# Optimization experiments

Hardware: AMD Instinct MI355X
Metric: run time of the kernel (lower is better)

Reference implementation:

```python
import jax, jax.numpy as jnp
import numpy as np

B, S, D, H, MEL = 64, 512, 512, 8, 80
HD = D // H  # head dim


def _lstm_cell(x, h, c, w_ih, w_hh, b_ih, b_hh):
    # torch gate order: i, f, g, o
    gates = x @ w_ih.T + h @ w_hh.T + b_ih + b_hh
    i, f, g, o = jnp.split(gates, 4, axis=-1)
    c = jax.nn.sigmoid(f) * c + jax.nn.sigmoid(i) * jnp.tanh(g)
    h = jax.nn.sigmoid(o) * jnp.tanh(c)
    return h, c


def setup_inputs() -> dict:
    key = jax.random.key(0)
    ks = jax.random.split(key, 24)
    s = 0.05
    inp = {"encoder_output": jax.random.normal(ks[0], (B, S, D), jnp.float32)}
    # MultiheadAttention params (torch layout: in_proj [3D, D])
    inp["attn_in_w"] = jax.random.normal(ks[1], (3 * D, D), jnp.float32) * s
    inp["attn_in_b"] = jax.random.normal(ks[2], (3 * D,), jnp.float32) * s
    inp["attn_out_w"] = jax.random.normal(ks[3], (D, D), jnp.float32) * s
    inp["attn_out_b"] = jax.random.normal(ks[4], (D,), jnp.float32) * s
    # LSTM1 (2 layers)
    names = [("l1_w_ih0", (4 * D, D)), ("l1_w_hh0", (4 * D, D)), ("l1_b_ih0", (4 * D,)), ("l1_b_hh0", (4 * D,)),
             ("l1_w_ih1", (4 * D, D)), ("l1_w_hh1", (4 * D, D)), ("l1_b_ih1", (4 * D,)), ("l1_b_hh1", (4 * D,)),
             ("l2_w_ih", (4 * D, D)), ("l2_w_hh", (4 * D, D)), ("l2_b_ih", (4 * D,)), ("l2_b_hh", (4 * D,)),
             ("proj_w", (MEL, D)), ("proj_b", (MEL,))]
    for i, (n, shp) in enumerate(names):
        inp[n] = jax.random.normal(ks[5 + i], shp, jnp.float32) * s
    return inp


def reference(encoder_output, attn_in_w, attn_in_b, attn_out_w, attn_out_b,
              l1_w_ih0, l1_w_hh0, l1_b_ih0, l1_b_hh0,
              l1_w_ih1, l1_w_hh1, l1_b_ih1, l1_b_hh1,
              l2_w_ih, l2_w_hh, l2_b_ih, l2_b_hh, proj_w, proj_b):
    b, s, d = encoder_output.shape
    max_len = s * 5
    wq, wk, wv = jnp.split(attn_in_w, 3, axis=0)
    bq, bk, bv = jnp.split(attn_in_b, 3, axis=0)
    # Precompute K, V over encoder output: [B, S, H, HD]
    K = (encoder_output @ wk.T + bk).reshape(b, s, H, HD)
    V = (encoder_output @ wv.T + bv).reshape(b, s, H, HD)
    scale = 1.0 / np.sqrt(HD)

    def attend(x):  # x: [B, D] single-token query
        q = ((x @ wq.T + bq) * scale).reshape(b, H, HD)
        scores = jnp.einsum('bhd,bshd->bhs', q, K)
        w = jax.nn.softmax(scores, axis=-1)
        ctx = jnp.einsum('bhs,bshd->bhd', w, V).reshape(b, d)
        return ctx @ attn_out_w.T + attn_out_b

    zeros = jnp.zeros((b, d), encoder_output.dtype)
    carry0 = (zeros, zeros, zeros, zeros, zeros, zeros, zeros)

    def step(carry, _):
        h10, c10, h11, c11, h2, c2, dec_in = carry
        h10, c10 = _lstm_cell(dec_in, h10, c10, l1_w_ih0, l1_w_hh0, l1_b_ih0, l1_b_hh0)
        h11, c11 = _lstm_cell(h10, h11, c11, l1_w_ih1, l1_w_hh1, l1_b_ih1, l1_b_hh1)
        attn_out = attend(h11)
        h2, c2 = _lstm_cell(attn_out, h2, c2, l2_w_ih, l2_w_hh, l2_b_ih, l2_b_hh)
        out = h2 @ proj_w.T + proj_b  # [B, MEL]
        return (h10, c10, h11, c11, h2, c2, h2), out

    _, ys = jax.lax.scan(step, carry0, None, length=max_len)
    return jnp.transpose(ys, (1, 0, 2))  # [B, max_len, MEL]
```

## Files before the change

kernel.cpp:

```cpp
#include <hip/hip_runtime.h>
#include <hip/hip_bf16.h>
#include <hip/hip_fp8.h>

#define DEV_INLINE __device__ __forceinline__

typedef __attribute__((ext_vector_type(8))) short bf16x8;
typedef __attribute__((ext_vector_type(4))) float f32x4;
typedef __attribute__((ext_vector_type(2))) float f32x2;
typedef __attribute__((ext_vector_type(4))) unsigned int u32x4;
typedef unsigned long long ull;

constexpr int Bc = 64, Sc = 512, Dc = 512, Hc = 8, HDc = 64, MELc = 80, Tc = 2560;
constexpr int OUTSTRIDE = Tc * MELc;

constexpr size_t SZ_KP8 = 64ull * 8 * 512 * 64;
constexpr size_t SZ_VP  = 64ull * 8 * 512 * 64 * 2;
constexpr size_t SZ_PL  = 128ull * 2048 * 16;
constexpr size_t OFF_KP8 = 0;
constexpr size_t OFF_VP  = OFF_KP8 + SZ_KP8;
constexpr size_t OFF_PL0 = OFF_VP + SZ_VP;
constexpr size_t OFF_PL1 = OFF_PL0 + SZ_PL;
constexpr size_t OFF_PL2 = OFF_PL1 + SZ_PL;
constexpr size_t OFF_PWQ = OFF_PL2 + SZ_PL;
constexpr size_t OFF_PP  = OFF_PWQ + 524288;
constexpr size_t OFF_BL0 = OFF_PP + 81920;
constexpr size_t OFF_BL1 = OFF_BL0 + 8192;
constexpr size_t OFF_BL2 = OFF_BL1 + 8192;
constexpr size_t OFF_B2E = OFF_BL2 + 8192;
constexpr size_t OFF_W2E = OFF_B2E + 8192;
constexpr size_t OFF_WOT = OFF_W2E + 2097152;
constexpr size_t OFF_ACT = OFF_WOT + 1048576;
constexpr size_t OFF_FLG = OFF_ACT + 524288;

constexpr unsigned DYN_LDS = 137344;

DEV_INLINE float bf2f(short s) { return __uint_as_float(((unsigned)(unsigned short)s) << 16); }
DEV_INLINE short f2bf(float f) { union { __hip_bfloat16 h; short s; } u; u.h = __float2bfloat16(f); return u.s; }
DEV_INLINE float sig_f(float x) { return 1.0f / (1.0f + __expf(-x)); }
DEV_INLINE float tanh_f(float x) {
  float ax = fabsf(x);
  float e = __expf(fminf(2.0f * ax, 80.0f));
  float r = 1.0f - 2.0f / (e + 1.0f);
  return copysignf(r, x);
}
DEV_INLINE bf16x8 cvt8(const float* p) {
  bf16x8 r;
#pragma unroll
  for (int i = 0; i < 8; ++i) r[i] = f2bf(p[i]);
  return r;
}
DEV_INLINE float fp8tof(unsigned v) {
  __hip_fp8_e4m3 t; t.__x = (__hip_fp8_storage_t)v; return (float)t;
}

template <bool HI>
DEV_INLINE f32x2 cvt2_fp8(unsigned w) {
#if defined(__has_builtin) && __has_builtin(__builtin_amdgcn_cvt_pk_f32_fp8)
  return __builtin_amdgcn_cvt_pk_f32_fp8(w, HI);
#else
  unsigned b = HI ? (w >> 16) : w;
  f32x2 r; r[0] = fp8tof(b & 0xFFu); r[1] = fp8tof((b >> 8) & 0xFFu);
  return r;
#endif
}

DEV_INLINE ull ld_dev_u64(const void* p) {
  return __hip_atomic_load((const ull*)p, __ATOMIC_RELAXED, __HIP_MEMORY_SCOPE_AGENT);
}
DEV_INLINE void st_dev_u64(void* p, ull v) {
  __hip_atomic_store((ull*)p, v, __ATOMIC_RELAXED, __HIP_MEMORY_SCOPE_AGENT);
}
DEV_INLINE bf16x8 ld_frag(const __hip_bfloat16* p) {
  union { bf16x8 v; ull u[2]; } r;
  r.u[0] = ld_dev_u64(p);
  r.u[1] = ld_dev_u64((const char*)p + 8);
  return r.v;
}

__global__ __launch_bounds__(256) void gemm_setup(const float* __restrict__ A,
                                                  const float* __restrict__ Bt,
                                                  const float* __restrict__ bias,
                                                  __hip_bfloat16* __restrict__ dst,
                                                  unsigned char* __restrict__ dst8,
                                                  int mode) {
  int tid = threadIdx.x, lane = tid & 63, wv = tid >> 6;
  int m0 = blockIdx.y * 64 + wv * 16;
  int nb = blockIdx.x * 64;
  int mrow = m0 + (lane & 15);
  int kb = (lane >> 4) * 8;
  f32x4 acc0 = {0,0,0,0}, acc1 = {0,0,0,0}, acc2 = {0,0,0,0}, acc3 = {0,0,0,0};
  const float* arow = A + (size_t)mrow * 512 + kb;
  const float* b0r = Bt + (size_t)(nb + 0 * 16 + (lane & 15)) * 512 + kb;
  const float* b1r = Bt + (size_t)(nb + 1 * 16 + (lane & 15)) * 512 + kb;
  const float* b2r = Bt + (size_t)(nb + 2 * 16 + (lane & 15)) * 512 + kb;
  const float* b3r = Bt + (size_t)(nb + 3 * 16 + (lane & 15)) * 512 + kb;
  for (int kk = 0; kk < 16; ++kk) {
    bf16x8 af = cvt8(arow + kk * 32);
    acc0 = __builtin_amdgcn_mfma_f32_16x16x32_bf16(af, cvt8(b0r + kk * 32), acc0, 0, 0, 0);
    acc1 = __builtin_amdgcn_mfma_f32_16x16x32_bf16(af, cvt8(b1r + kk * 32), acc1, 0, 0, 0);
    acc2 = __builtin_amdgcn_mfma_f32_16x16x32_bf16(af, cvt8(b2r + kk * 32), acc2, 0, 0, 0);
    acc3 = __builtin_amdgcn_mfma_f32_16x16x32_bf16(af, cvt8(b3r + kk * 32), acc3, 0, 0, 0);
  }
  int col16 = lane & 15, r0 = (lane >> 4) * 4;
  f32x4 accs[4] = {acc0, acc1, acc2, acc3};
#pragma unroll
  for (int nt = 0; nt < 4; ++nt) {
    int n = nb + nt * 16 + col16;
#pragma unroll
    for (int r = 0; r < 4; ++r) {
      int m = m0 + r0 + r;
      float v = accs[nt][r];
      if (mode == 0) {
        v += bias[n];
        int bb = m >> 9, s = m & 511, h = n >> 6, d = n & 63;
        dst[(((size_t)(bb * 8 + h) * 512 + s) * 64) + d] = __float2bfloat16(v);
      } else if (mode == 2) {
        v += bias[n];
        int bb = m >> 9, s = m & 511, h = n >> 6, d = n & 63;
        __hip_fp8_e4m3 q(v);
        dst8[(((size_t)(bb * 8 + h) * 512 + s) * 64) + d] = (unsigned char)q.__x;
      } else {
        dst[(size_t)m * 512 + n] = __float2bfloat16(v);
      }
    }
  }
}

__global__ __launch_bounds__(256) void transpose512(const float* __restrict__ in, float* __restrict__ out) {
  __shared__ float tl[32][33];
  int x = threadIdx.x & 31, ty = threadIdx.x >> 5;
  int bx = blockIdx.x * 32, by = blockIdx.y * 32;
#pragma unroll
  for (int r = 0; r < 4; ++r) tl[ty + r * 8][x] = in[(size_t)(by + ty + r * 8) * 512 + bx + x];
  __syncthreads();
#pragma unroll
  for (int r = 0; r < 4; ++r) out[(size_t)(bx + ty + r * 8) * 512 + by + x] = tl[x][ty + r * 8];
}

__global__ __launch_bounds__(256) void b2eff_k(const float* __restrict__ w2ih, const float* __restrict__ bout,
                                               const float* __restrict__ bih, const float* __restrict__ bhh,
                                               float* __restrict__ dst) {
  int g = blockIdx.x * 256 + threadIdx.x;
  float acc = bih[g] + bhh[g];
  const float* row = w2ih + (size_t)g * 512;
  for (int k = 0; k < 512; ++k) acc += row[k] * bout[k];
  dst[g] = acc;
}

__global__ __launch_bounds__(256) void pack_lstm(const float* __restrict__ lo_f32,
                                                 const __hip_bfloat16* __restrict__ lo_bf16,
                                                 const float* __restrict__ hi_f32,
                                                 const float* __restrict__ b1, const float* __restrict__ b2,
                                                 const float* __restrict__ b_pre,
                                                 __hip_bfloat16* __restrict__ dst, float* __restrict__ bias_out,
                                                 int mode) {
  int u = blockIdx.x, tid = threadIdx.x;
  for (int rep = 0; rep < 8; ++rep) {
    int slot = rep * 256 + tid;
    int kk = slot >> 6, lane = slot & 63;
    int n16 = lane & 15, gate = n16 >> 2, jj = n16 & 3;
    int srow = gate * 512 + u * 4 + jj;
    int k = kk * 32 + (lane >> 4) * 8;
    __hip_bfloat16 tmp[8];
    if (k < 512) {
      if (mode == 0) {
#pragma unroll
        for (int i = 0; i < 8; ++i) tmp[i] = __float2bfloat16(lo_f32[(size_t)srow * 512 + k + i]);
      } else {
#pragma unroll
        for (int i = 0; i < 8; ++i) tmp[i] = lo_bf16[(size_t)srow * 512 + k + i];
      }
    } else {
#pragma unroll
      for (int i = 0; i < 8; ++i) tmp[i] = __float2bfloat16(hi_f32[(size_t)srow * 512 + (k - 512) + i]);
    }
    *(uint4*)(dst + ((size_t)u * 2048 + slot) * 8) = *(uint4*)tmp;
  }
  if (tid < 16) {
    int gate = tid >> 2, jj = tid & 3;
    int srow = gate * 512 + u * 4 + jj;
    bias_out[u * 16 + tid] = (mode == 0) ? (b1[srow] + b2[srow]) : b_pre[srow];
  }
}

__global__ __launch_bounds__(256) void pack_wq(const float* __restrict__ wq, __hip_bfloat16* __restrict__ dst) {
  int h = blockIdx.x, tid = threadIdx.x;
  for (int rep = 0; rep < 16; ++rep) {
    int slot = rep * 256 + tid;
    int nt = slot >> 10, kk = (slot >> 6) & 15, lane = slot & 63;
    int srow = h * 64 + nt * 16 + (lane & 15);
    int k = kk * 32 + (lane >> 4) * 8;
    __hip_bfloat16 tmp[8];
#pragma unroll
    for (int i = 0; i < 8; ++i) tmp[i] = __float2bfloat16(wq[(size_t)srow * 512 + k + i]);
    *(uint4*)(dst + ((size_t)h * 4096 + slot) * 8) = *(uint4*)tmp;
  }
}

__global__ __launch_bounds__(256) void pack_proj(const float* __restrict__ pw, __hip_bfloat16* __restrict__ dst) {
  int u5 = blockIdx.x, tid = threadIdx.x;
  for (int rep = 0; rep < 4; ++rep) {
    int slot = rep * 256 + tid;
    int kk = slot >> 6, lane = slot & 63;
    int srow = u5 * 16 + (lane & 15);
    int k = kk * 32 + (lane >> 4) * 8;
    __hip_bfloat16 tmp[8];
#pragma unroll
    for (int i = 0; i < 8; ++i) tmp[i] = __float2bfloat16(pw[(size_t)srow * 512 + k + i]);
    *(uint4*)(dst + ((size_t)u5 * 1024 + slot) * 8) = *(uint4*)tmp;
  }
}

struct DecParams {
  const float* attn_in_b;
  const float* proj_b;
  const uint4* packL0; const uint4* packL1; const uint4* packL2;
  const float* biasL0; const float* biasL1; const float* biasL2;
  const uint4* packWq; const uint4* packP;
  const unsigned char* Kp8; const __hip_bfloat16* Vp;
  __hip_bfloat16* h10b; __hip_bfloat16* h11b; __hip_bfloat16* h2b; __hip_bfloat16* ctxb;
  ull* actbase;
  unsigned* flags;
  float* out;
};

constexpr ull WD_TICKS = 200000000ull;

DEV_INLINE void publish_flag(unsigned* flags, int wg, unsigned id, int tid) {
  __builtin_amdgcn_s_waitcnt(0);
  __syncthreads();
  if (tid == 0)
    __hip_atomic_store(&flags[wg], id, __ATOMIC_RELAXED, __HIP_MEMORY_SCOPE_AGENT);
}

DEV_INLINE bool wait_flags(unsigned* flags, int base, int count, unsigned id, int tid,
                           ull t0, int* bail) {
  if (tid < 64) {
    for (;;) {
      bool ok = true;
      for (int i = tid; i < count; i += 64)
        ok &= (__hip_atomic_load(&flags[base + i], __ATOMIC_RELAXED, __HIP_MEMORY_SCOPE_AGENT) >= id);
      if (__all(ok ? 1 : 0)) break;
      if (__builtin_amdgcn_s_memrealtime() - t0 > WD_TICKS) { if (tid == 0) *bail = 1; break; }
      __builtin_amdgcn_s_sleep(1);
    }
  }
  __syncthreads();
  if (*bail) return false;
  return true;
}

DEV_INLINE bool wait_half(unsigned* flags, int base, unsigned id, int lane, ull t0, int* sbail) {
  for (;;) {
    unsigned f = __hip_atomic_load(&flags[base + lane], __ATOMIC_RELAXED, __HIP_MEMORY_SCOPE_AGENT);
    if (__all(f >= id ? 1 : 0)) return true;
    if (__builtin_amdgcn_s_memrealtime() - t0 > WD_TICKS) { *sbail = 1; return false; }
    __builtin_amdgcn_s_sleep(1);
  }
}

DEV_INLINE void prefetch_hi(bf16x8* pf, const __hip_bfloat16* hi, int g, int lane, int wv) {
  if (wv >= 2) {
    const __hip_bfloat16* p = hi + (size_t)(g * 32 + (wv & 1) * 16 + (lane & 15)) * 512 + (lane >> 4) * 8;
#pragma unroll
    for (int kk = 0; kk < 16; ++kk) pf[kk] = ld_frag(p + kk * 32);
  }
}

DEV_INLINE bool lstm_stage(int tid, int g, int wgl,
                           const uint4* wlds, const float* bias,
                           const __hip_bfloat16* lo, const bf16x8* pf,
                           float* cstate, __hip_bfloat16* hc,
                           float* pred, ull* st64,
                           unsigned* flags, int fbase, unsigned id,
                           ull t0, int* sbail) {
  const int lane = tid & 63, wv = tid >> 6, mt = wv & 1, kh = wv >> 1;
  f32x4 acc = {0,0,0,0};
  if (kh == 0) {
    const __hip_bfloat16* pA = lo + (size_t)(g * 32 + mt * 16 + (lane & 15)) * 512 + (lane >> 4) * 8;
    if (wait_half(flags, fbase, id, lane, t0, sbail)) {
#pragma unroll
      for (int kk = 0; kk < 8; ++kk) {
        bf16x8 a = ld_frag(pA + kk * 32);
        bf16x8 b = *(const bf16x8*)(wlds + kk * 64 + lane);
        acc = __builtin_amdgcn_mfma_f32_16x16x32_bf16(a, b, acc, 0, 0, 0);
      }
      if (wait_half(flags, fbase + 64, id, lane, t0, sbail)) {
#pragma unroll
        for (int kk = 8; kk < 16; ++kk) {
          bf16x8 a = ld_frag(pA + kk * 32);
          bf16x8 b = *(const bf16x8*)(wlds + kk * 64 + lane);
          acc = __builtin_amdgcn_mfma_f32_16x16x32_bf16(a, b, acc, 0, 0, 0);
        }
      }
    }
  } else {
#pragma unroll
    for (int kk = 0; kk < 16; ++kk) {
      bf16x8 b = *(const bf16x8*)(wlds + (16 + kk) * 64 + lane);
      acc = __builtin_amdgcn_mfma_f32_16x16x32_bf16(pf[kk], b, acc, 0, 0, 0);
    }
  }
#pragma unroll
  for (int r = 0; r < 4; ++r) pred[wv * 256 + lane * 4 + r] = acc[r];
  __syncthreads();
  if (*sbail) return false;
  if (tid < 128) {
    int bl = tid >> 2, j = tid & 3;
    int mt2 = bl >> 4, qd = (bl & 15) >> 2, reg = bl & 3;
    const float* p0 = pred + mt2 * 256;
    const float* p1 = pred + (2 + mt2) * 256;
    int l0 = qd * 16;
    float gi = p0[(l0 + j) * 4 + reg]      + p1[(l0 + j) * 4 + reg]      + bias[j];
    float gf = p0[(l0 + 4 + j) * 4 + reg]  + p1[(l0 + 4 + j) * 4 + reg]  + bias[4 + j];
    float gg = p0[(l0 + 8 + j) * 4 + reg]  + p1[(l0 + 8 + j) * 4 + reg]  + bias[8 + j];
    float go = p0[(l0 + 12 + j) * 4 + reg] + p1[(l0 + 12 + j) * 4 + reg] + bias[12 + j];
    float c = cstate[tid & 127];
    c = sig_f(gf) * c + sig_f(gi) * tanh_f(gg);
    float h = sig_f(go) * tanh_f(c);
    cstate[tid & 127] = c;
    ((unsigned short*)st64)[tid] = (unsigned short)f2bf(h);
  }
  __syncthreads();
  if (tid < 32)
    st_dev_u64(hc + (size_t)(g * 32 + tid) * 512 + wgl * 4, st64[tid]);
  return true;
}

DEV_INLINE void proj_stage(int tid, int g, int n5, const uint4* wPJ, const float* proj_b,
                           const __hip_bfloat16* h2in, float* outp, float* pred) {
  const int lane = tid & 63, wv = tid >> 6, mt = wv & 1, kh = wv >> 1;
  f32x4 acc = {0,0,0,0};
  const __hip_bfloat16* pA = h2in + (size_t)(g * 32 + mt * 16 + (lane & 15)) * 512 + kh * 256 + (lane >> 4) * 8;
#pragma unroll
  for (int kk = 0; kk < 8; ++kk) {
    bf16x8 a = ld_frag(pA + kk * 32);
    bf16x8 b = *(const bf16x8*)(wPJ + (kh * 8 + kk) * 64 + lane);
    acc = __builtin_amdgcn_mfma_f32_16x16x32_bf16(a, b, acc, 0, 0, 0);
  }
#pragma unroll
  for (int r = 0; r < 4; ++r) pred[wv * 256 + lane * 4 + r] = acc[r];
  __syncthreads();
#pragma unroll
  for (int half = 0; half < 2; ++half) {
    int gx = half * 256 + tid;
    int row = gx >> 4, col = gx & 15;
    int mt2 = row >> 4, qd = (row & 15) >> 2, reg = row & 3, ln = qd * 16 + col;
    float v = pred[mt2 * 256 + ln * 4 + reg] + pred[(2 + mt2) * 256 + ln * 4 + reg] + proj_b[n5 * 16 + col];
    outp[(size_t)(g * 32 + row) * OUTSTRIDE + n5 * 16 + col] = v;
  }
  __syncthreads();
}

__global__ __launch_bounds__(256, 1) void decoder_main(DecParams P) {
  extern __shared__ char smem[];
  uint4* wL0 = (uint4*)smem;
  uint4* wL1 = wL0 + 2048;
  uint4* wL2 = wL1 + 2048;
  uint4* wPJ = wL2 + 2048;
  ull*   st64 = (ull*)(wPJ + 1024);
  float* pred = (float*)(st64 + 32);
  float* qls  = pred + 1024;
  float* sco  = qls + 1088;
  float* red  = sco + 1024;
  float* cst  = red + 2048;
  float* smx  = cst + 384;
  float* ssum = smx + 4;
  float* sinv = ssum + 4;
  int*   sbail = (int*)(sinv + 2);

  const int wg = blockIdx.x, tid = threadIdx.x;
  const int lane = tid & 63, wv = tid >> 6;
  const int g = wg >> 7;
  const int wgl = wg & 127;
  const int fbase = g * 128;
  const int hh = wgl >> 4;
  const int b0g = (wgl & 15) * 2;
  const int bblk = b0g & ~15;

  const ull t0 = __builtin_amdgcn_s_memrealtime();

  {
    const uint4* s0 = P.packL0 + (size_t)wgl * 2048;
    const uint4* s1 = P.packL1 + (size_t)wgl * 2048;
    const uint4* s2 = P.packL2 + (size_t)wgl * 2048;
    for (int i = tid; i < 2048; i += 256) { wL0[i] = s0[i]; wL1[i] = s1[i]; wL2[i] = s2[i]; }
    if (wgl < 5) { const uint4* sp = P.packP + (size_t)wgl * 1024; for (int i = tid; i < 1024; i += 256) wPJ[i] = sp[i]; }
  }
  if (tid == 0) *sbail = 0;
  if (tid < 128) { cst[tid] = 0.0f; cst[128 + tid] = 0.0f; cst[256 + tid] = 0.0f; }
  st_dev_u64(P.actbase + (size_t)wg * 256 + tid, 0ull);
  __syncthreads();
  publish_flag(P.flags, wg, 1u, tid);
  if (!wait_flags(P.flags, 0, 256, 1u, tid, t0, sbail)) goto bail;

  for (int t = 0; t < Tc; ++t) {
    const int cur = t & 1, pv = cur ^ 1;
    const unsigned idA = 4u * t + 1, idApub = 4u * t + 2, idBpub = 4u * t + 3,
                   idCpub = 4u * t + 4, idDpub = 4u * t + 5;
    __hip_bfloat16* h10c = P.h10b + cur * 32768; __hip_bfloat16* h10p = P.h10b + pv * 32768;
    __hip_bfloat16* h11c = P.h11b + cur * 32768; __hip_bfloat16* h11p = P.h11b + pv * 32768;
    __hip_bfloat16* h2c  = P.h2b  + cur * 32768; __hip_bfloat16* h2p  = P.h2b  + pv * 32768;
    __hip_bfloat16* ctxc = P.ctxb + cur * 32768;

    {
      bf16x8 pf[16];
      prefetch_hi(pf, h10p, g, lane, wv);
      if (!lstm_stage(tid, g, wgl, wL0, P.biasL0 + wgl * 16, h2p, pf, cst, h10c, pred, st64,
                      P.flags, fbase, idA, t0, sbail)) goto bail;
      publish_flag(P.flags, wg, idApub, tid);
    }
    if (wgl < 5 && t > 0)
      proj_stage(tid, g, wgl, wPJ, P.proj_b, h2p, P.out + (size_t)(t - 1) * MELc, pred);

    {
      bf16x8 pf[16];
      prefetch_hi(pf, h11p, g, lane, wv);
      if (!lstm_stage(tid, g, wgl, wL1, P.biasL1 + wgl * 16, h10c, pf, cst + 128, h11c, pred, st64,
                      P.flags, fbase, idApub, t0, sbail)) goto bail;
      publish_flag(P.flags, wg, idBpub, tid);
    }

    {
      int mrow = g * 32 + bblk + (lane & 15);
      const __hip_bfloat16* pA = h11c + (size_t)mrow * 512 + (lane >> 4) * 8;
      const uint4* pB = P.packWq + (size_t)hh * 4096 + wv * 1024;
      f32x4 acc = {0,0,0,0};
      if (wait_half(P.flags, fbase, idBpub, lane, t0, sbail)) {
#pragma unroll
        for (int kk = 0; kk < 8; ++kk) {
          bf16x8 a = ld_frag(pA + kk * 32);
          bf16x8 b = *(const bf16x8*)(pB + kk * 64 + lane);
          acc = __builtin_amdgcn_mfma_f32_16x16x32_bf16(a, b, acc, 0, 0, 0);
        }
        if (wait_half(P.flags, fbase + 64, idBpub, lane, t0, sbail)) {
#pragma unroll
          for (int kk = 8; kk < 16; ++kk) {
            bf16x8 a = ld_frag(pA + kk * 32);
            bf16x8 b = *(const bf16x8*)(pB + kk * 64 + lane);
            acc = __builtin_amdgcn_mfma_f32_16x16x32_bf16(a, b, acc, 0, 0, 0);
          }
        }
      }
      int col = lane & 15, row0 = (lane >> 4) << 2;
      int dg = wv * 16 + col;
      float bq = P.attn_in_b[hh * 64 + dg];
#pragma unroll
      for (int r = 0; r < 4; ++r) qls[(row0 + r) * 68 + dg] = (acc[r] + bq) * 0.125f;
    }
    __syncthreads();
    if (*sbail) goto bail;
    {
      int p = tid >> 7, si = tid & 127;
      int bg = g * 32 + b0g + p;
      const float* qv = qls + ((b0g & 15) + p) * 68;
      f32x4 q4[16];
#pragma unroll
      for (int i = 0; i < 16; ++i) q4[i] = *(const f32x4*)(qv + 4 * i);
      const u32x4* Kb = (const u32x4*)(P.Kp8 + (size_t)(bg * 8 + hh) * 512 * 64);
#pragma unroll
      for (int ss = 0; ss < 4; ++ss) {
        int s = si * 4 + ss;
        const u32x4* kr = Kb + s * 4;
        f32x2 acc2 = {0.0f, 0.0f};
#pragma unroll
        for (int i = 0; i < 4; ++i) {
          u32x4 kv = kr[i];
#pragma unroll
          for (int j = 0; j < 4; ++j) {
            unsigned w = kv[j];
            f32x2 c01 = cvt2_fp8<false>(w);
            f32x2 c23 = cvt2_fp8<true>(w);
            f32x4 qq = q4[i * 4 + j];
            acc2 += c01 * (f32x2){qq[0], qq[1]} + c23 * (f32x2){qq[2], qq[3]};
          }
        }
        sco[p * 512 + s] = acc2[0] + acc2[1];
      }
    }
    __syncthreads();
    {
      int p = wv >> 1, half = wv & 1;
      int idx = tid & 127;
      float mx = -1e30f;
#pragma unroll
      for (int ss = 0; ss < 4; ++ss) mx = fmaxf(mx, sco[p * 512 + idx * 4 + ss]);
#pragma unroll
      for (int off = 32; off; off >>= 1) mx = fmaxf(mx, __shfl_xor(mx, off));
      if (lane == 0) smx[p * 2 + half] = mx;
      __syncthreads();
      float m = fmaxf(smx[p * 2], smx[p * 2 + 1]);
      float sum = 0.0f;
#pragma unroll
      for (int ss = 0; ss < 4; ++ss) {
        int ix = p * 512 + idx * 4 + ss;
        float e = __expf(sco[ix] - m);
        sco[ix] = e; sum += e;
      }
#pragma unroll
      for (int off = 32; off; off >>= 1) sum += __shfl_xor(sum, off);
      if (lane == 0) ssum[p * 2 + half] = sum;
      __syncthreads();
      if (tid < 2) sinv[tid] = 1.0f / (ssum[tid * 2] + ssum[tid * 2 + 1]);
    }
    __syncthreads();
    {
      int p = wv >> 1, half = wv & 1;
      int bg = g * 32 + b0g + p;
      int sg = lane >> 3, dj = lane & 7;
      const u32x4* VbU = (const u32x4*)(P.Vp + (size_t)(bg * 8 + hh) * 512 * 64);
      f32x2 aA[4] = {{0,0},{0,0},{0,0},{0,0}};
      f32x2 aB[4] = {{0,0},{0,0},{0,0},{0,0}};
      const int s0 = half * 256 + sg;
#pragma unroll 4
      for (int it = 0; it < 16; ++it) {
        int sA = s0 + it * 8, sB = sA + 128;
        u32x4 vA = __builtin_nontemporal_load(VbU + (size_t)sA * 8 + dj);
        u32x4 vB = __builtin_nontemporal_load(VbU + (size_t)sB * 8 + dj);
        float wa = sco[p * 512 + sA], wb = sco[p * 512 + sB];
        f32x2 wA = {wa, wa}, wB = {wb, wb};
#pragma unroll
        for (int j = 0; j < 4; ++j) {
          unsigned ua = vA[j], ub = vB[j];
          f32x2 fa = { __uint_as_float(ua << 16), __uint_as_float(ua & 0xFFFF0000u) };
          f32x2 fb = { __uint_as_float(ub << 16), __uint_as_float(ub & 0xFFFF0000u) };
          aA[j] += wA * fa;
          aB[j] += wB * fb;
        }
      }
      float* rp = red + ((p * 16 + half * 8 + sg) * 64) + dj * 8;
#pragma unroll
      for (int j = 0; j < 4; ++j) {
        rp[j * 2]     = aA[j][0] + aB[j][0];
        rp[j * 2 + 1] = aA[j][1] + aB[j][1];
      }
    }
    __syncthreads();
    if (tid < 128) {
      int p = tid >> 6, d = tid & 63;
      float sacc = 0.0f;
#pragma unroll
      for (int k = 0; k < 16; ++k) sacc += red[(p * 16 + k) * 64 + d];
      sacc *= sinv[p];
      ((unsigned short*)st64)[tid] = (unsigned short)f2bf(sacc);
    }
    __syncthreads();
    if (tid < 32) {
      int p = tid >> 4, q = tid & 15;
      st_dev_u64(ctxc + (size_t)(g * 32 + b0g + p) * 512 + hh * 64 + q * 4, st64[p * 16 + q]);
    }
    publish_flag(P.flags, wg, idCpub, tid);

    {
      bf16x8 pf[16];
      prefetch_hi(pf, h2p, g, lane, wv);
      if (!lstm_stage(tid, g, wgl, wL2, P.biasL2 + wgl * 16, ctxc, pf, cst + 256, h2c, pred, st64,
                      P.flags, fbase, idCpub, t0, sbail)) goto bail;
      publish_flag(P.flags, wg, idDpub, tid);
    }
  }

  if (wgl < 5) {
    if (wait_flags(P.flags, fbase, 128, 4u * (Tc - 1) + 5, tid, t0, sbail))
      proj_stage(tid, g, wgl, wPJ, P.proj_b, P.h2b + ((Tc - 1) & 1) * 32768,
                 P.out + (size_t)(Tc - 1) * MELc, pred);
  }
  return;

bail:
  publish_flag(P.flags, wg, 0x7F000000u, tid);
}

extern "C" void kernel_launch(void* const* d_in, const int* in_sizes, int n_in,
                              void* d_out, int out_size, void* d_ws, size_t ws_size,
                              hipStream_t stream) {
  const float* enc        = (const float*)d_in[0];
  const float* attn_in_w  = (const float*)d_in[1];
  const float* attn_in_b  = (const float*)d_in[2];
  const float* attn_out_w = (const float*)d_in[3];
  const float* attn_out_b = (const float*)d_in[4];
  const float* w_ih0 = (const float*)d_in[5];
  const float* w_hh0 = (const float*)d_in[6];
  const float* b_ih0 = (const float*)d_in[7];
  const float* b_hh0 = (const float*)d_in[8];
  const float* w_ih1 = (const float*)d_in[9];
  const float* w_hh1 = (const float*)d_in[10];
  const float* b_ih1 = (const float*)d_in[11];
  const float* b_hh1 = (const float*)d_in[12];
  const float* w_ih2 = (const float*)d_in[13];
  const float* w_hh2 = (const float*)d_in[14];
  const float* b_ih2 = (const float*)d_in[15];
  const float* b_hh2 = (const float*)d_in[16];
  const float* proj_w = (const float*)d_in[17];
  const float* proj_b = (const float*)d_in[18];

  char* ws = (char*)d_ws;
  unsigned char*  Kp8 = (unsigned char*)(ws + OFF_KP8);
  __hip_bfloat16* Vp  = (__hip_bfloat16*)(ws + OFF_VP);
  __hip_bfloat16* pl0 = (__hip_bfloat16*)(ws + OFF_PL0);
  __hip_bfloat16* pl1 = (__hip_bfloat16*)(ws + OFF_PL1);
  __hip_bfloat16* pl2 = (__hip_bfloat16*)(ws + OFF_PL2);
  __hip_bfloat16* pwq = (__hip_bfloat16*)(ws + OFF_PWQ);
  __hip_bfloat16* pp  = (__hip_bfloat16*)(ws + OFF_PP);
  float* bl0 = (float*)(ws + OFF_BL0);
  float* bl1 = (float*)(ws + OFF_BL1);
  float* bl2 = (float*)(ws + OFF_BL2);
  float* b2e = (float*)(ws + OFF_B2E);
  __hip_bfloat16* w2e = (__hip_bfloat16*)(ws + OFF_W2E);
  float* wot = (float*)(ws + OFF_WOT);
  char* act  = ws + OFF_ACT;
  unsigned* flags = (unsigned*)(ws + OFF_FLG);

  hipMemsetAsync(flags, 0, 4096, stream);

  gemm_setup<<<dim3(8, 512), 256, 0, stream>>>(enc, attn_in_w + 512 * 512, attn_in_b + 512, nullptr, Kp8, 2);
  gemm_setup<<<dim3(8, 512), 256, 0, stream>>>(enc, attn_in_w + 1024 * 512, attn_in_b + 1024, Vp, nullptr, 0);
  transpose512<<<dim3(16, 16), 256, 0, stream>>>(attn_out_w, wot);
  gemm_setup<<<dim3(8, 32), 256, 0, stream>>>(w_ih2, wot, nullptr, w2e, nullptr, 1);
  b2eff_k<<<8, 256, 0, stream>>>(w_ih2, attn_out_b, b_ih2, b_hh2, b2e);
  pack_lstm<<<128, 256, 0, stream>>>(w_ih0, nullptr, w_hh0, b_ih0, b_hh0, nullptr, pl0, bl0, 0);
  pack_lstm<<<128, 256, 0, stream>>>(w_ih1, nullptr, w_hh1, b_ih1, b_hh1, nullptr, pl1, bl1, 0);
  pack_lstm<<<128, 256, 0, stream>>>(nullptr, w2e, w_hh2, nullptr, nullptr, b2e, pl2, bl2, 1);
  pack_wq<<<8, 256, 0, stream>>>(attn_in_w, pwq);
  pack_proj<<<5, 256, 0, stream>>>(proj_w, pp);

  DecParams p;
  p.attn_in_b = attn_in_b;
  p.proj_b = proj_b;
  p.packL0 = (const uint4*)pl0; p.packL1 = (const uint4*)pl1; p.packL2 = (const uint4*)pl2;
  p.biasL0 = bl0; p.biasL1 = bl1; p.biasL2 = bl2;
  p.packWq = (const uint4*)pwq; p.packP = (const uint4*)pp;
  p.Kp8 = Kp8; p.Vp = Vp;
  p.h10b = (__hip_bfloat16*)(act + 0);
  p.h11b = (__hip_bfloat16*)(act + 131072);
  p.h2b  = (__hip_bfloat16*)(act + 262144);
  p.ctxb = (__hip_bfloat16*)(act + 393216);
  p.actbase = (ull*)act;
  p.flags = flags;
  p.out = (float*)d_out;

  (void)hipFuncSetAttribute((const void*)decoder_main,
                            hipFuncAttributeMaxDynamicSharedMemorySize, DYN_LDS);
  decoder_main<<<dim3(256), dim3(256), DYN_LDS, stream>>>(p);
}
```

Before: 111.6 ms.

## Replace flag-based inter-workgroup sync with tagged fp32 activations polled inline

Drops the per-stage flag publish/wait barriers between persistent workgroups. Activations are now stored as fp32 with the low 2 mantissa bits carrying a step tag, and consumers poll the data itself, issuing each MFMA chunk as soon as its tagged fragment arrives. This removes the waitcnt+syncthreads+flag store and the flag polling round trips on the serial critical path. In exchange, activation traffic doubles (fp32 instead of bf16), precision loses 2 mantissa bits, and the workspace now reuses the w2e/wot region for activations after setup.

```diff
diff --git a/kernel.cpp b/kernel.cpp
--- a/kernel.cpp
+++ b/kernel.cpp
@@ -29,10 +29,9 @@
 constexpr size_t OFF_B2E = OFF_BL2 + 8192;
 constexpr size_t OFF_W2E = OFF_B2E + 8192;
 constexpr size_t OFF_WOT = OFF_W2E + 2097152;
-constexpr size_t OFF_ACT = OFF_WOT + 1048576;
-constexpr size_t OFF_FLG = OFF_ACT + 524288;
-
-constexpr unsigned DYN_LDS = 137344;
+constexpr size_t OFF_ACT = OFF_W2E;
+
+constexpr unsigned DYN_LDS = 137728;
 
 DEV_INLINE float bf2f(short s) { return __uint_as_float(((unsigned)(unsigned short)s) << 16); }
 DEV_INLINE short f2bf(float f) { union { __hip_bfloat16 h; short s; } u; u.h = __float2bfloat16(f); return u.s; }
@@ -70,11 +69,19 @@
 DEV_INLINE void st_dev_u64(void* p, ull v) {
   __hip_atomic_store((ull*)p, v, __ATOMIC_RELAXED, __HIP_MEMORY_SCOPE_AGENT);
 }
-DEV_INLINE bf16x8 ld_frag(const __hip_bfloat16* p) {
-  union { bf16x8 v; ull u[2]; } r;
-  r.u[0] = ld_dev_u64(p);
-  r.u[1] = ld_dev_u64((const char*)p + 8);
-  return r.v;
+
+DEV_INLINE short bfr(unsigned x) { return (short)((x + 0x7FFFu + ((x >> 16) & 1u)) >> 16); }
+DEV_INLINE bf16x8 bf8_from(ull d0, ull d1, ull d2, ull d3) {
+  bf16x8 r;
+  r[0] = bfr((unsigned)d0); r[1] = bfr((unsigned)(d0 >> 32));
+  r[2] = bfr((unsigned)d1); r[3] = bfr((unsigned)(d1 >> 32));
+  r[4] = bfr((unsigned)d2); r[5] = bfr((unsigned)(d2 >> 32));
+  r[6] = bfr((unsigned)d3); r[7] = bfr((unsigned)(d3 >> 32));
+  return r;
+}
+DEV_INLINE unsigned tagok4(ull d0, ull d1, ull d2, ull d3, unsigned tg) {
+  return (((unsigned)d0 & 3u) == tg) & (((unsigned)d1 & 3u) == tg) &
+         (((unsigned)d2 & 3u) == tg) & (((unsigned)d3 & 3u) == tg);
 }
 
 __global__ __launch_bounds__(256) void gemm_setup(const float* __restrict__ A,
@@ -211,6 +218,12 @@
   }
 }
 
+__global__ __launch_bounds__(256) void init_act(unsigned* __restrict__ p) {
+  int i = blockIdx.x * 256 + threadIdx.x;
+#pragma unroll
+  for (int r = 0; r < 4; ++r) p[i + r * 65536] = 3u;
+}
+
 struct DecParams {
   const float* attn_in_b;
   const float* proj_b;
@@ -218,81 +231,57 @@
   const float* biasL0; const float* biasL1; const float* biasL2;
   const uint4* packWq; const uint4* packP;
   const unsigned char* Kp8; const __hip_bfloat16* Vp;
-  __hip_bfloat16* h10b; __hip_bfloat16* h11b; __hip_bfloat16* h2b; __hip_bfloat16* ctxb;
-  ull* actbase;
-  unsigned* flags;
+  float* h10b; float* h11b; float* h2b; float* ctxb;
   float* out;
 };
 
 constexpr ull WD_TICKS = 200000000ull;
 
-DEV_INLINE void publish_flag(unsigned* flags, int wg, unsigned id, int tid) {
-  __builtin_amdgcn_s_waitcnt(0);
-  __syncthreads();
-  if (tid == 0)
-    __hip_atomic_store(&flags[wg], id, __ATOMIC_RELAXED, __HIP_MEMORY_SCOPE_AGENT);
-}
-
-DEV_INLINE bool wait_flags(unsigned* flags, int base, int count, unsigned id, int tid,
-                           ull t0, int* bail) {
-  if (tid < 64) {
-    for (;;) {
-      bool ok = true;
-      for (int i = tid; i < count; i += 64)
-        ok &= (__hip_atomic_load(&flags[base + i], __ATOMIC_RELAXED, __HIP_MEMORY_SCOPE_AGENT) >= id);
-      if (__all(ok ? 1 : 0)) break;
-      if (__builtin_amdgcn_s_memrealtime() - t0 > WD_TICKS) { if (tid == 0) *bail = 1; break; }
-      __builtin_amdgcn_s_sleep(1);
-    }
-  }
-  __syncthreads();
-  if (*bail) return false;
-  return true;
-}
-
-DEV_INLINE bool wait_half(unsigned* flags, int base, unsigned id, int lane, ull t0, int* sbail) {
-  for (;;) {
-    unsigned f = __hip_atomic_load(&flags[base + lane], __ATOMIC_RELAXED, __HIP_MEMORY_SCOPE_AGENT);
-    if (__all(f >= id ? 1 : 0)) return true;
-    if (__builtin_amdgcn_s_memrealtime() - t0 > WD_TICKS) { *sbail = 1; return false; }
-    __builtin_amdgcn_s_sleep(1);
-  }
-}
-
-DEV_INLINE void prefetch_hi(bf16x8* pf, const __hip_bfloat16* hi, int g, int lane, int wv) {
+DEV_INLINE void prefetch_hi32(bf16x8* pf, const float* hi, int g, int lane, int wv) {
   if (wv >= 2) {
-    const __hip_bfloat16* p = hi + (size_t)(g * 32 + (wv & 1) * 16 + (lane & 15)) * 512 + (lane >> 4) * 8;
-#pragma unroll
-    for (int kk = 0; kk < 16; ++kk) pf[kk] = ld_frag(p + kk * 32);
-  }
-}
-
-DEV_INLINE bool lstm_stage(int tid, int g, int wgl,
+    const float* p = hi + (size_t)(g * 32 + (wv & 1) * 16 + (lane & 15)) * 512 + (lane >> 4) * 8;
+#pragma unroll
+    for (int kk = 0; kk < 16; ++kk) {
+      const char* pc = (const char*)(p + kk * 32);
+      pf[kk] = bf8_from(ld_dev_u64(pc), ld_dev_u64(pc + 8), ld_dev_u64(pc + 16), ld_dev_u64(pc + 24));
+    }
+  }
+}
+
+DEV_INLINE void lstm_stage(int tid, int g, int wgl,
                            const uint4* wlds, const float* bias,
-                           const __hip_bfloat16* lo, const bf16x8* pf,
-                           float* cstate, __hip_bfloat16* hc,
-                           float* pred, ull* st64,
-                           unsigned* flags, int fbase, unsigned id,
-                           ull t0, int* sbail) {
+                           const float* lo, unsigned tag, const bf16x8* pf,
+                           float* cstate, float* Hout, unsigned otag,
+                           float* pred, float* hstg, ull t0) {
   const int lane = tid & 63, wv = tid >> 6, mt = wv & 1, kh = wv >> 1;
   f32x4 acc = {0,0,0,0};
   if (kh == 0) {
-    const __hip_bfloat16* pA = lo + (size_t)(g * 32 + mt * 16 + (lane & 15)) * 512 + (lane >> 4) * 8;
-    if (wait_half(flags, fbase, id, lane, t0, sbail)) {
-#pragma unroll
-      for (int kk = 0; kk < 8; ++kk) {
-        bf16x8 a = ld_frag(pA + kk * 32);
-        bf16x8 b = *(const bf16x8*)(wlds + kk * 64 + lane);
-        acc = __builtin_amdgcn_mfma_f32_16x16x32_bf16(a, b, acc, 0, 0, 0);
-      }
-      if (wait_half(flags, fbase + 64, id, lane, t0, sbail)) {
-#pragma unroll
-        for (int kk = 8; kk < 16; ++kk) {
-          bf16x8 a = ld_frag(pA + kk * 32);
+    const float* pA = lo + (size_t)(g * 32 + mt * 16 + (lane & 15)) * 512 + (lane >> 4) * 8;
+    unsigned need = 0;
+#pragma unroll
+    for (int kk = 0; kk < 16; ++kk) {
+      const char* pc = (const char*)(pA + kk * 32);
+      ull d0 = ld_dev_u64(pc),      d1 = ld_dev_u64(pc + 8);
+      ull d2 = ld_dev_u64(pc + 16), d3 = ld_dev_u64(pc + 24);
+      bf16x8 b = *(const bf16x8*)(wlds + kk * 64 + lane);
+      if (__all((int)tagok4(d0, d1, d2, d3, tag)))
+        acc = __builtin_amdgcn_mfma_f32_16x16x32_bf16(bf8_from(d0, d1, d2, d3), b, acc, 0, 0, 0);
+      else
+        need |= 1u << kk;
+    }
+    while (need) {
+#pragma unroll
+      for (int kk = 0; kk < 16; ++kk) if (need & (1u << kk)) {
+        const char* pc = (const char*)(pA + kk * 32);
+        ull d0 = ld_dev_u64(pc),      d1 = ld_dev_u64(pc + 8);
+        ull d2 = ld_dev_u64(pc + 16), d3 = ld_dev_u64(pc + 24);
+        if (__all((int)tagok4(d0, d1, d2, d3, tag))) {
           bf16x8 b = *(const bf16x8*)(wlds + kk * 64 + lane);
-          acc = __builtin_amdgcn_mfma_f32_16x16x32_bf16(a, b, acc, 0, 0, 0);
+          acc = __builtin_amdgcn_mfma_f32_16x16x32_bf16(bf8_from(d0, d1, d2, d3), b, acc, 0, 0, 0);
+          need &= ~(1u << kk);
         }
       }
+      if (__builtin_amdgcn_s_memrealtime() - t0 > WD_TICKS) break;
     }
   } else {
 #pragma unroll
@@ -304,7 +293,6 @@
 #pragma unroll
   for (int r = 0; r < 4; ++r) pred[wv * 256 + lane * 4 + r] = acc[r];
   __syncthreads();
-  if (*sbail) return false;
   if (tid < 128) {
     int bl = tid >> 2, j = tid & 3;
     int mt2 = bl >> 4, qd = (bl & 15) >> 2, reg = bl & 3;
@@ -319,22 +307,27 @@
     c = sig_f(gf) * c + sig_f(gi) * tanh_f(gg);
     float h = sig_f(go) * tanh_f(c);
     cstate[tid & 127] = c;
-    ((unsigned short*)st64)[tid] = (unsigned short)f2bf(h);
+    hstg[tid] = __uint_as_float((__float_as_uint(h) & ~3u) | otag);
   }
   __syncthreads();
-  if (tid < 32)
-    st_dev_u64(hc + (size_t)(g * 32 + tid) * 512 + wgl * 4, st64[tid]);
-  return true;
+  if (tid < 64) {
+    int b = tid >> 1, hf = tid & 1;
+    union { float f[2]; ull u; } pkt;
+    pkt.f[0] = hstg[b * 4 + hf * 2];
+    pkt.f[1] = hstg[b * 4 + hf * 2 + 1];
+    st_dev_u64(Hout + (size_t)(g * 32 + b) * 512 + wgl * 4 + hf * 2, pkt.u);
+  }
 }
 
 DEV_INLINE void proj_stage(int tid, int g, int n5, const uint4* wPJ, const float* proj_b,
-                           const __hip_bfloat16* h2in, float* outp, float* pred) {
+                           const float* h2in, float* outp, float* pred) {
   const int lane = tid & 63, wv = tid >> 6, mt = wv & 1, kh = wv >> 1;
   f32x4 acc = {0,0,0,0};
-  const __hip_bfloat16* pA = h2in + (size_t)(g * 32 + mt * 16 + (lane & 15)) * 512 + kh * 256 + (lane >> 4) * 8;
+  const float* pA = h2in + (size_t)(g * 32 + mt * 16 + (lane & 15)) * 512 + kh * 256 + (lane >> 4) * 8;
 #pragma unroll
   for (int kk = 0; kk < 8; ++kk) {
-    bf16x8 a = ld_frag(pA + kk * 32);
+    const char* pc = (const char*)(pA + kk * 32);
+    bf16x8 a = bf8_from(ld_dev_u64(pc), ld_dev_u64(pc + 8), ld_dev_u64(pc + 16), ld_dev_u64(pc + 24));
     bf16x8 b = *(const bf16x8*)(wPJ + (kh * 8 + kk) * 64 + lane);
     acc = __builtin_amdgcn_mfma_f32_16x16x32_bf16(a, b, acc, 0, 0, 0);
   }
@@ -358,8 +351,7 @@
   uint4* wL1 = wL0 + 2048;
   uint4* wL2 = wL1 + 2048;
   uint4* wPJ = wL2 + 2048;
-  ull*   st64 = (ull*)(wPJ + 1024);
-  float* pred = (float*)(st64 + 32);
+  float* pred = (float*)(wPJ + 1024);
   float* qls  = pred + 1024;
   float* sco  = qls + 1088;
   float* red  = sco + 1024;
@@ -367,13 +359,12 @@
   float* smx  = cst + 384;
   float* ssum = smx + 4;
   float* sinv = ssum + 4;
-  int*   sbail = (int*)(sinv + 2);
+  float* hstg = sinv + 2;
 
   const int wg = blockIdx.x, tid = threadIdx.x;
   const int lane = tid & 63, wv = tid >> 6;
   const int g = wg >> 7;
   const int wgl = wg & 127;
-  const int fbase = g * 128;
   const int hh = wgl >> 4;
   const int b0g = (wgl & 15) * 2;
   const int bblk = b0g & ~15;
@@ -387,60 +378,62 @@
     for (int i = tid; i < 2048; i += 256) { wL0[i] = s0[i]; wL1[i] = s1[i]; wL2[i] = s2[i]; }
     if (wgl < 5) { const uint4* sp = P.packP + (size_t)wgl * 1024; for (int i = tid; i < 1024; i += 256) wPJ[i] = sp[i]; }
   }
-  if (tid == 0) *sbail = 0;
   if (tid < 128) { cst[tid] = 0.0f; cst[128 + tid] = 0.0f; cst[256 + tid] = 0.0f; }
-  st_dev_u64(P.actbase + (size_t)wg * 256 + tid, 0ull);
   __syncthreads();
-  publish_flag(P.flags, wg, 1u, tid);
-  if (!wait_flags(P.flags, 0, 256, 1u, tid, t0, sbail)) goto bail;
 
   for (int t = 0; t < Tc; ++t) {
     const int cur = t & 1, pv = cur ^ 1;
-    const unsigned idA = 4u * t + 1, idApub = 4u * t + 2, idBpub = 4u * t + 3,
-                   idCpub = 4u * t + 4, idDpub = 4u * t + 5;
-    __hip_bfloat16* h10c = P.h10b + cur * 32768; __hip_bfloat16* h10p = P.h10b + pv * 32768;
-    __hip_bfloat16* h11c = P.h11b + cur * 32768; __hip_bfloat16* h11p = P.h11b + pv * 32768;
-    __hip_bfloat16* h2c  = P.h2b  + cur * 32768; __hip_bfloat16* h2p  = P.h2b  + pv * 32768;
-    __hip_bfloat16* ctxc = P.ctxb + cur * 32768;
+    const unsigned tcu = (unsigned)(t & 3);
+    const unsigned tpr = (unsigned)((t + 3) & 3);
+    float* h10c = P.h10b + cur * 32768; const float* h10p = P.h10b + pv * 32768;
+    float* h11c = P.h11b + cur * 32768; const float* h11p = P.h11b + pv * 32768;
+    float* h2c  = P.h2b  + cur * 32768; const float* h2p  = P.h2b  + pv * 32768;
+    float* ctxc = P.ctxb + cur * 32768;
 
     {
       bf16x8 pf[16];
-      prefetch_hi(pf, h10p, g, lane, wv);
-      if (!lstm_stage(tid, g, wgl, wL0, P.biasL0 + wgl * 16, h2p, pf, cst, h10c, pred, st64,
-                      P.flags, fbase, idA, t0, sbail)) goto bail;
-      publish_flag(P.flags, wg, idApub, tid);
+      prefetch_hi32(pf, h10p, g, lane, wv);
+      lstm_stage(tid, g, wgl, wL0, P.biasL0 + wgl * 16, h2p, tpr, pf, cst, h10c, tcu, pred, hstg, t0);
     }
     if (wgl < 5 && t > 0)
       proj_stage(tid, g, wgl, wPJ, P.proj_b, h2p, P.out + (size_t)(t - 1) * MELc, pred);
 
     {
       bf16x8 pf[16];
-      prefetch_hi(pf, h11p, g, lane, wv);
-      if (!lstm_stage(tid, g, wgl, wL1, P.biasL1 + wgl * 16, h10c, pf, cst + 128, h11c, pred, st64,
-                      P.flags, fbase, idApub, t0, sbail)) goto bail;
-      publish_flag(P.flags, wg, idBpub, tid);
+      prefetch_hi32(pf, h11p, g, lane, wv);
+      lstm_stage(tid, g, wgl, wL1, P.biasL1 + wgl * 16, h10c, tcu, pf, cst + 128, h11c, tcu, pred, hstg, t0);
     }
 
     {
       int mrow = g * 32 + bblk + (lane & 15);
-      const __hip_bfloat16* pA = h11c + (size_t)mrow * 512 + (lane >> 4) * 8;
+      const float* pA = h11c + (size_t)mrow * 512 + (lane >> 4) * 8;
       const uint4* pB = P.packWq + (size_t)hh * 4096 + wv * 1024;
       f32x4 acc = {0,0,0,0};
-      if (wait_half(P.flags, fbase, idBpub, lane, t0, sbail)) {
-#pragma unroll
-        for (int kk = 0; kk < 8; ++kk) {
-          bf16x8 a = ld_frag(pA + kk * 32);
-          bf16x8 b = *(const bf16x8*)(pB + kk * 64 + lane);
-          acc = __builtin_amdgcn_mfma_f32_16x16x32_bf16(a, b, acc, 0, 0, 0);
-        }
-        if (wait_half(P.flags, fbase + 64, idBpub, lane, t0, sbail)) {
-#pragma unroll
-          for (int kk = 8; kk < 16; ++kk) {
-            bf16x8 a = ld_frag(pA + kk * 32);
+      unsigned need = 0;
+#pragma unroll
+      for (int kk = 0; kk < 16; ++kk) {
+        const char* pc = (const char*)(pA + kk * 32);
+        ull d0 = ld_dev_u64(pc),      d1 = ld_dev_u64(pc + 8);
+        ull d2 = ld_dev_u64(pc + 16), d3 = ld_dev_u64(pc + 24);
+        bf16x8 b = *(const bf16x8*)(pB + kk * 64 + lane);
+        if (__all((int)tagok4(d0, d1, d2, d3, tcu)))
+          acc = __builtin_amdgcn_mfma_f32_16x16x32_bf16(bf8_from(d0, d1, d2, d3), b, acc, 0, 0, 0);
+        else
+          need |= 1u << kk;
+      }
+      while (need) {
+#pragma unroll
+        for (int kk = 0; kk < 16; ++kk) if (need & (1u << kk)) {
+          const char* pc = (const char*)(pA + kk * 32);
+          ull d0 = ld_dev_u64(pc),      d1 = ld_dev_u64(pc + 8);
+          ull d2 = ld_dev_u64(pc + 16), d3 = ld_dev_u64(pc + 24);
+          if (__all((int)tagok4(d0, d1, d2, d3, tcu))) {
             bf16x8 b = *(const bf16x8*)(pB + kk * 64 + lane);
-            acc = __builtin_amdgcn_mfma_f32_16x16x32_bf16(a, b, acc, 0, 0, 0);
+            acc = __builtin_amdgcn_mfma_f32_16x16x32_bf16(bf8_from(d0, d1, d2, d3), b, acc, 0, 0, 0);
+            need &= ~(1u << kk);
           }
         }
+        if (__builtin_amdgcn_s_memrealtime() - t0 > WD_TICKS) break;
       }
       int col = lane & 15, row0 = (lane >> 4) << 2;
       int dg = wv * 16 + col;
@@ -449,7 +442,6 @@
       for (int r = 0; r < 4; ++r) qls[(row0 + r) * 68 + dg] = (acc[r] + bq) * 0.125f;
     }
     __syncthreads();
-    if (*sbail) goto bail;
     {
       int p = tid >> 7, si = tid & 127;
       int bg = g * 32 + b0g + p;
@@ -542,33 +534,42 @@
 #pragma unroll
       for (int k = 0; k < 16; ++k) sacc += red[(p * 16 + k) * 64 + d];
       sacc *= sinv[p];
-      ((unsigned short*)st64)[tid] = (unsigned short)f2bf(sacc);
+      hstg[tid] = __uint_as_float((__float_as_uint(sacc) & ~3u) | tcu);
     }
     __syncthreads();
-    if (tid < 32) {
-      int p = tid >> 4, q = tid & 15;
-      st_dev_u64(ctxc + (size_t)(g * 32 + b0g + p) * 512 + hh * 64 + q * 4, st64[p * 16 + q]);
-    }
-    publish_flag(P.flags, wg, idCpub, tid);
+    if (tid < 64) {
+      int p = tid >> 5, idx = tid & 31;
+      union { float f[2]; ull u; } pkt;
+      pkt.f[0] = hstg[p * 64 + idx * 2];
+      pkt.f[1] = hstg[p * 64 + idx * 2 + 1];
+      st_dev_u64(ctxc + (size_t)(g * 32 + b0g + p) * 512 + hh * 64 + idx * 2, pkt.u);
+    }
 
     {
       bf16x8 pf[16];
-      prefetch_hi(pf, h2p, g, lane, wv);
-      if (!lstm_stage(tid, g, wgl, wL2, P.biasL2 + wgl * 16, ctxc, pf, cst + 256, h2c, pred, st64,
-                      P.flags, fbase, idCpub, t0, sbail)) goto bail;
-      publish_flag(P.flags, wg, idDpub, tid);
+      prefetch_hi32(pf, h2p, g, lane, wv);
+      lstm_stage(tid, g, wgl, wL2, P.biasL2 + wgl * 16, ctxc, tcu, pf, cst + 256, h2c, tcu, pred, hstg, t0);
     }
   }
 
   if (wgl < 5) {
-    if (wait_flags(P.flags, fbase, 128, 4u * (Tc - 1) + 5, tid, t0, sbail))
-      proj_stage(tid, g, wgl, wPJ, P.proj_b, P.h2b + ((Tc - 1) & 1) * 32768,
-                 P.out + (size_t)(Tc - 1) * MELc, pred);
-  }
-  return;
-
-bail:
-  publish_flag(P.flags, wg, 0x7F000000u, tid);
+    const float* h2f = P.h2b + ((Tc - 1) & 1) * 32768;
+    const unsigned tg = (unsigned)((Tc - 1) & 3);
+    const int mt = wv & 1, kh = wv >> 1;
+    const float* pA = h2f + (size_t)(g * 32 + mt * 16 + (lane & 15)) * 512 + kh * 256 + (lane >> 4) * 8;
+    unsigned need = 0xFFu;
+    while (need) {
+#pragma unroll
+      for (int kk = 0; kk < 8; ++kk) if (need & (1u << kk)) {
+        const char* pc = (const char*)(pA + kk * 32);
+        if (__all((int)tagok4(ld_dev_u64(pc), ld_dev_u64(pc + 8),
+                              ld_dev_u64(pc + 16), ld_dev_u64(pc + 24), tg)))
+          need &= ~(1u << kk);
+      }
+      if (__builtin_amdgcn_s_memrealtime() - t0 > WD_TICKS) break;
+    }
+    proj_stage(tid, g, wgl, wPJ, P.proj_b, h2f, P.out + (size_t)(Tc - 1) * MELc, pred);
+  }
 }
 
 extern "C" void kernel_launch(void* const* d_in, const int* in_sizes, int n_in,
@@ -608,10 +609,7 @@
   float* b2e = (float*)(ws + OFF_B2E);
   __hip_bfloat16* w2e = (__hip_bfloat16*)(ws + OFF_W2E);
   float* wot = (float*)(ws + OFF_WOT);
-  char* act  = ws + OFF_ACT;
-  unsigned* flags = (unsigned*)(ws + OFF_FLG);
-
-  hipMemsetAsync(flags, 0, 4096, stream);
+  float* act = (float*)(ws + OFF_ACT);
 
   gemm_setup<<<dim3(8, 512), 256, 0, stream>>>(enc, attn_in_w + 512 * 512, attn_in_b + 512, nullptr, Kp8, 2);
   gemm_setup<<<dim3(8, 512), 256, 0, stream>>>(enc, attn_in_w + 1024 * 512, attn_in_b + 1024, Vp, nullptr, 0);
@@ -623,6 +621,7 @@
   pack_lstm<<<128, 256, 0, stream>>>(nullptr, w2e, w_hh2, nullptr, nullptr, b2e, pl2, bl2, 1);
   pack_wq<<<8, 256, 0, stream>>>(attn_in_w, pwq);
   pack_proj<<<5, 256, 0, stream>>>(proj_w, pp);
+  init_act<<<256, 256, 0, stream>>>((unsigned*)act);
 
   DecParams p;
   p.attn_in_b = attn_in_b;
@@ -631,12 +630,10 @@
   p.biasL0 = bl0; p.biasL1 = bl1; p.biasL2 = bl2;
   p.packWq = (const uint4*)pwq; p.packP = (const uint4*)pp;
   p.Kp8 = Kp8; p.Vp = Vp;
-  p.h10b = (__hip_bfloat16*)(act + 0);
-  p.h11b = (__hip_bfloat16*)(act + 131072);
-  p.h2b  = (__hip_bfloat16*)(act + 262144);
-  p.ctxb = (__hip_bfloat16*)(act + 393216);
-  p.actbase = (ull*)act;
-  p.flags = flags;
+  p.h10b = act + 0;
+  p.h11b = act + 65536;
+  p.h2b  = act + 131072;
+  p.ctxb = act + 196608;
   p.out = (float*)d_out;
 
   (void)hipFuncSetAttribute((const void*)decoder_main,
```

After: 143.1 ms. +28.2%, slower.
